# Kernel tuning notes

Measured on AMD Instinct MI355X. Metric: run time of the kernel, lower is better.

## Reference

```python
import jax, jax.numpy as jnp
import numpy as np

EMBED_DIM = 1024
SEQ_LEN = 4096
NUM_HEADS = 16
HEAD_DIM = EMBED_DIM // NUM_HEADS
FREQ_BINS = SEQ_LEN // 2 + 1  # 2049
LN_EPS = 1e-5


def setup_inputs() -> dict:
    key = jax.random.key(0)
    ks = jax.random.split(key, 12)
    B = 4
    x = jax.random.normal(ks[0], (B, SEQ_LEN, EMBED_DIM), dtype=jnp.float32)
    # LayerNorm affine params
    ln_w = jnp.ones((EMBED_DIM,), dtype=jnp.float32)
    ln_b = jnp.zeros((EMBED_DIM,), dtype=jnp.float32)
    # spectral base filter / bias: (H, freq_bins, 1)
    base_filter = jax.random.normal(ks[1], (NUM_HEADS, FREQ_BINS, 1), dtype=jnp.float32)
    base_bias = jax.random.normal(ks[2], (NUM_HEADS, FREQ_BINS, 1), dtype=jnp.float32) - 0.1
    # adaptive MLP (depth=2, width=embed_dim): D -> D -> D -> H*freq*2, relu hidden
    out_size = NUM_HEADS * FREQ_BINS * 2
    s0 = 1.0 / np.sqrt(EMBED_DIM)
    w0 = jax.random.uniform(ks[3], (EMBED_DIM, EMBED_DIM), jnp.float32, -s0, s0)
    b0 = jax.random.uniform(ks[4], (EMBED_DIM,), jnp.float32, -s0, s0)
    w1 = jax.random.uniform(ks[5], (EMBED_DIM, EMBED_DIM), jnp.float32, -s0, s0)
    b1 = jax.random.uniform(ks[6], (EMBED_DIM,), jnp.float32, -s0, s0)
    w2 = jax.random.uniform(ks[7], (EMBED_DIM, out_size), jnp.float32, -s0, s0)
    b2 = jax.random.uniform(ks[8], (out_size,), jnp.float32, -s0, s0)
    return {"x": x, "ln_w": ln_w, "ln_b": ln_b,
            "base_filter": base_filter, "base_bias": base_bias,
            "w0": w0, "b0": b0, "w1": w1, "b1": b1, "w2": w2, "b2": b2}


def _complex_activation(z):
    mag = jnp.abs(z)
    scale = jax.nn.gelu(mag) / (mag + 1e-6)
    return z * scale


def reference(x, ln_w, ln_b, base_filter, base_bias, w0, b0, w1, b1, w2, b2):
    B, N, D = x.shape  # N == SEQ_LEN, D == EMBED_DIM
    # pre-norm LayerNorm over last dim
    mu = x.mean(axis=-1, keepdims=True)
    var = x.var(axis=-1, keepdims=True)
    x_norm = (x - mu) / jnp.sqrt(var + LN_EPS) * ln_w + ln_b
    # split heads: (B, H, N, head_dim)
    x_heads = x_norm.reshape(B, N, NUM_HEADS, HEAD_DIM).transpose(0, 2, 1, 3)
    F_fft = jnp.fft.rfft(x_heads, axis=2)  # (B, H, freq, head_dim), complex
    # adaptive params from mean-pooled context
    context = x_norm.mean(axis=1)  # (B, D)
    h = jax.nn.relu(context @ w0 + b0)
    h = jax.nn.relu(h @ w1 + b1)
    adapt = h @ w2 + b2  # (B, H*freq*2)
    adapt = adapt.reshape(B, NUM_HEADS, FREQ_BINS, 2)
    adaptive_scale = adapt[..., 0:1]
    adaptive_bias = adapt[..., 1:2]
    effective_filter = base_filter * (1.0 + adaptive_scale)  # (B, H, freq, 1)
    effective_bias = base_bias + adaptive_bias
    F_mod = F_fft * effective_filter + effective_bias
    F_nl = _complex_activation(F_mod)
    x_filt = jnp.fft.irfft(F_nl, n=SEQ_LEN, axis=2)  # (B, H, N, head_dim)
    x_filt = x_filt.transpose(0, 2, 1, 3).reshape(B, SEQ_LEN, EMBED_DIM)
    return x_filt  # dropout is identity (inference / rate 0)
```

## Files before the change

kernel.cpp:

```cpp
#include <hip/hip_runtime.h>
#include <hip/hip_fp16.h>
#include <math.h>

#define B_ 4
#define N_ 4096
#define D_ 1024
#define H_ 16
#define HD_ 64
#define FB_ 2049

typedef unsigned short ushort_t;
typedef unsigned int uint_t;

__device__ __forceinline__ float2 cmul(float2 a, float2 b) {
    return make_float2(a.x*b.x - a.y*b.y, a.x*b.y + a.y*b.x);
}
__device__ __forceinline__ float2 cadd(float2 a, float2 b){return make_float2(a.x+b.x,a.y+b.y);}
__device__ __forceinline__ float2 csub(float2 a, float2 b){return make_float2(a.x-b.x,a.y-b.y);}
__device__ __forceinline__ float2 cconj(float2 a){return make_float2(a.x,-a.y);}
__device__ __forceinline__ float2 addi(float2 a, float2 b){return make_float2(a.x-b.y, a.y+b.x);}
__device__ __forceinline__ float2 subi(float2 a, float2 b){return make_float2(a.x+b.y, a.y-b.x);}

__device__ __forceinline__ float gelu_t(float m) {
    float u = 0.7978845608028654f * (m + 0.044715f * m * m * m);
    float e = __expf(-2.0f * u);
    float th = (1.0f - e) / (1.0f + e);
    return 0.5f * m * (1.0f + th);
}
__device__ __forceinline__ float2 cact(float2 z) {
    float m = sqrtf(z.x*z.x + z.y*z.y);
    float s = gelu_t(m) / (m + 1e-6f);
    return make_float2(z.x*s, z.y*s);
}

__device__ __forceinline__ ushort_t f2h(float f) {
    __half h = __float2half_rn(f);
    return *reinterpret_cast<ushort_t*>(&h);
}
__device__ __forceinline__ float h2f(ushort_t u) {
    __half h = *reinterpret_cast<__half*>(&u);
    return __half2float(h);
}
__device__ __forceinline__ uint_t pk2(float a, float b) {
    return (uint_t)f2h(a) | ((uint_t)f2h(b) << 16);
}
__device__ __forceinline__ float lo_f(uint_t u){ return h2f((ushort_t)(u & 0xffffu)); }
__device__ __forceinline__ float hi_f(uint_t u){ return h2f((ushort_t)(u >> 16)); }

#define IX(e) ((e) + ((e) >> 4))

__device__ __forceinline__ int rev12(int p) {
    return ((p & 7) << 9) | (((p >> 3) & 7) << 6) | (((p >> 6) & 7) << 3) | ((p >> 9) & 7);
}

__global__ __launch_bounds__(256) void k_normT(const float* __restrict__ x,
                                               const float* __restrict__ lnw,
                                               const float* __restrict__ lnb,
                                               ushort_t* __restrict__ xt,
                                               float* __restrict__ cpart) {
    __shared__ ushort_t lds16[32 * 1032];
    uint_t* lds32 = (uint_t*)lds16;
    int blk = blockIdx.x;
    int b = blk >> 7, chunk = blk & 127;
    int n0 = chunk << 5;
    int lane = threadIdx.x & 63, w = threadIdx.x >> 6;
    const float4* lw4 = (const float4*)lnw;
    const float4* lb4 = (const float4*)lnb;
    float4 W0 = lw4[lane], W1 = lw4[lane+64], W2 = lw4[lane+128], W3 = lw4[lane+192];
    float4 G0 = lb4[lane], G1 = lb4[lane+64], G2 = lb4[lane+128], G3 = lb4[lane+192];

    for (int j = 0; j < 8; j++) {
        int r = (w << 3) + j;
        const float4* xr = (const float4*)(x + ((size_t)b * N_ + n0 + r) * D_);
        float4 v0 = xr[lane], v1 = xr[lane+64], v2 = xr[lane+128], v3 = xr[lane+192];
        float s = v0.x+v0.y+v0.z+v0.w + v1.x+v1.y+v1.z+v1.w
                + v2.x+v2.y+v2.z+v2.w + v3.x+v3.y+v3.z+v3.w;
        float q = v0.x*v0.x+v0.y*v0.y+v0.z*v0.z+v0.w*v0.w
                + v1.x*v1.x+v1.y*v1.y+v1.z*v1.z+v1.w*v1.w
                + v2.x*v2.x+v2.y*v2.y+v2.z*v2.z+v2.w*v2.w
                + v3.x*v3.x+v3.y*v3.y+v3.z*v3.z+v3.w*v3.w;
        for (int o = 1; o < 64; o <<= 1) { s += __shfl_xor(s, o); q += __shfl_xor(q, o); }
        float mu = s * (1.0f / D_);
        float rstd = rsqrtf(q * (1.0f / D_) - mu * mu + 1e-5f);
        int base = r * 516 + 2 * lane;
        lds32[base]       = pk2((v0.x-mu)*rstd*W0.x+G0.x, (v0.y-mu)*rstd*W0.y+G0.y);
        lds32[base + 1]   = pk2((v0.z-mu)*rstd*W0.z+G0.z, (v0.w-mu)*rstd*W0.w+G0.w);
        lds32[base + 128] = pk2((v1.x-mu)*rstd*W1.x+G1.x, (v1.y-mu)*rstd*W1.y+G1.y);
        lds32[base + 129] = pk2((v1.z-mu)*rstd*W1.z+G1.z, (v1.w-mu)*rstd*W1.w+G1.w);
        lds32[base + 256] = pk2((v2.x-mu)*rstd*W2.x+G2.x, (v2.y-mu)*rstd*W2.y+G2.y);
        lds32[base + 257] = pk2((v2.z-mu)*rstd*W2.z+G2.z, (v2.w-mu)*rstd*W2.w+G2.w);
        lds32[base + 384] = pk2((v3.x-mu)*rstd*W3.x+G3.x, (v3.y-mu)*rstd*W3.y+G3.y);
        lds32[base + 385] = pk2((v3.z-mu)*rstd*W3.z+G3.z, (v3.w-mu)*rstd*W3.w+G3.w);
    }
    __syncthreads();
    for (int half = 0; half < 2; half++) {
        int dp = threadIdx.x + (half << 8);
        float cs_e = 0.f, cs_o = 0.f;
        uint_t ce[16], co[16];
        #pragma unroll
        for (int i = 0; i < 16; i++) {
            uint_t w0 = lds32[(2*i) * 516 + dp];
            uint_t w1 = lds32[(2*i+1) * 516 + dp];
            ce[i] = (w0 & 0xffffu) | (w1 << 16);
            co[i] = (w0 >> 16) | (w1 & 0xffff0000u);
            cs_e += lo_f(w0) + lo_f(w1);
            cs_o += hi_f(w0) + hi_f(w1);
        }
        int de = dp * 2;
        uint4* dste = (uint4*)(xt + ((size_t)(b * 1024 + de)) * 4096 + n0);
        dste[0] = make_uint4(ce[0], ce[1], ce[2], ce[3]);
        dste[1] = make_uint4(ce[4], ce[5], ce[6], ce[7]);
        dste[2] = make_uint4(ce[8], ce[9], ce[10], ce[11]);
        dste[3] = make_uint4(ce[12], ce[13], ce[14], ce[15]);
        uint4* dsto = (uint4*)(xt + ((size_t)(b * 1024 + de + 1)) * 4096 + n0);
        dsto[0] = make_uint4(co[0], co[1], co[2], co[3]);
        dsto[1] = make_uint4(co[4], co[5], co[6], co[7]);
        dsto[2] = make_uint4(co[8], co[9], co[10], co[11]);
        dsto[3] = make_uint4(co[12], co[13], co[14], co[15]);
        ((float2*)(cpart + ((size_t)(b * 128 + chunk)) * D_))[dp] = make_float2(cs_e, cs_o);
    }
}

__global__ __launch_bounds__(256) void k_ctx(const float* __restrict__ cpart,
                                             float* __restrict__ ctx) {
    int id = blockIdx.x * 256 + threadIdx.x;
    int b = id >> 10, d = id & 1023;
    float s = 0.f;
    const float* p = cpart + (size_t)b * 128 * D_ + d;
    #pragma unroll 8
    for (int g = 0; g < 128; g++) s += p[g * D_];
    ctx[id] = s * (1.0f / N_);
}

__global__ __launch_bounds__(256) void k_mlp_part(const float* __restrict__ in,
                                                  const float* __restrict__ w,
                                                  float* __restrict__ part) {
    __shared__ float li[4 * 64];
    int ks = blockIdx.y;
    if (threadIdx.x < 256) {
        int i = threadIdx.x;
        int b = i >> 6, kk = i & 63;
        li[i] = in[b * 1024 + ks * 64 + kk];
    }
    __syncthreads();
    int col = blockIdx.x * 64 + (threadIdx.x & 63);
    int b = threadIdx.x >> 6;
    const float* wp = w + (size_t)(ks * 64) * 1024 + col;
    const float* ip = li + b * 64;
    float a0 = 0.f, a1 = 0.f, a2 = 0.f, a3 = 0.f;
    #pragma unroll
    for (int k = 0; k < 64; k += 4) {
        a0 = fmaf(ip[k],     wp[(size_t)k * 1024],        a0);
        a1 = fmaf(ip[k + 1], wp[(size_t)(k + 1) * 1024],  a1);
        a2 = fmaf(ip[k + 2], wp[(size_t)(k + 2) * 1024],  a2);
        a3 = fmaf(ip[k + 3], wp[(size_t)(k + 3) * 1024],  a3);
    }
    part[((size_t)ks * 4 + b) * 1024 + col] = (a0 + a1) + (a2 + a3);
}

__global__ __launch_bounds__(256) void k_mlp_part2(const float* __restrict__ part,
                                                   const float* __restrict__ bias,
                                                   const float* __restrict__ w,
                                                   float* __restrict__ part2) {
    __shared__ float li[4 * 64];
    int ks = blockIdx.y;
    if (threadIdx.x < 256) {
        int i = threadIdx.x;
        int b = i >> 6, kk = ks * 64 + (i & 63);
        float v = bias[kk];
        #pragma unroll
        for (int s = 0; s < 16; s++) v += part[((size_t)s * 4 + b) * 1024 + kk];
        li[i] = fmaxf(v, 0.f);
    }
    __syncthreads();
    int col = blockIdx.x * 64 + (threadIdx.x & 63);
    int b = threadIdx.x >> 6;
    const float* wp = w + (size_t)(ks * 64) * 1024 + col;
    const float* ip = li + b * 64;
    float a0 = 0.f, a1 = 0.f, a2 = 0.f, a3 = 0.f;
    #pragma unroll
    for (int k = 0; k < 64; k += 4) {
        a0 = fmaf(ip[k],     wp[(size_t)k * 1024],        a0);
        a1 = fmaf(ip[k + 1], wp[(size_t)(k + 1) * 1024],  a1);
        a2 = fmaf(ip[k + 2], wp[(size_t)(k + 2) * 1024],  a2);
        a3 = fmaf(ip[k + 3], wp[(size_t)(k + 3) * 1024],  a3);
    }
    part2[((size_t)ks * 4 + b) * 1024 + col] = (a0 + a1) + (a2 + a3);
}

__global__ __launch_bounds__(256) void k_adapt_part(const float* __restrict__ part2,
                                                    const float* __restrict__ b1,
                                                    const float* __restrict__ w2,
                                                    float* __restrict__ part3) {
    __shared__ float lh[4 * 128];
    int ks = blockIdx.y;
    for (int i = threadIdx.x; i < 512; i += 256) {
        int b = i >> 7, kk = (i & 127) + ks * 128;
        float v = b1[kk];
        #pragma unroll
        for (int s = 0; s < 16; s++) v += part2[((size_t)s * 4 + b) * 1024 + kk];
        lh[i] = fmaxf(v, 0.f);
    }
    __syncthreads();
    int j4 = blockIdx.x * 1024 + threadIdx.x * 4;
    if (j4 < 65568) {
        float a0x=0,a0y=0,a0z=0,a0w=0, a1x=0,a1y=0,a1z=0,a1w=0;
        float a2x=0,a2y=0,a2z=0,a2w=0, a3x=0,a3y=0,a3z=0,a3w=0;
        const float* wp = w2 + (size_t)(ks * 128) * 65568 + j4;
        #pragma unroll 4
        for (int k = 0; k < 128; k++) {
            float4 wv = *(const float4*)(wp + (size_t)k * 65568);
            float h0 = lh[k], h1 = lh[128 + k], h2 = lh[256 + k], h3 = lh[384 + k];
            a0x = fmaf(h0, wv.x, a0x); a0y = fmaf(h0, wv.y, a0y);
            a0z = fmaf(h0, wv.z, a0z); a0w = fmaf(h0, wv.w, a0w);
            a1x = fmaf(h1, wv.x, a1x); a1y = fmaf(h1, wv.y, a1y);
            a1z = fmaf(h1, wv.z, a1z); a1w = fmaf(h1, wv.w, a1w);
            a2x = fmaf(h2, wv.x, a2x); a2y = fmaf(h2, wv.y, a2y);
            a2z = fmaf(h2, wv.z, a2z); a2w = fmaf(h2, wv.w, a2w);
            a3x = fmaf(h3, wv.x, a3x); a3y = fmaf(h3, wv.y, a3y);
            a3z = fmaf(h3, wv.z, a3z); a3w = fmaf(h3, wv.w, a3w);
        }
        float* p3 = part3 + (size_t)ks * 4 * 65568 + j4;
        *(float4*)(p3)              = make_float4(a0x, a0y, a0z, a0w);
        *(float4*)(p3 + 65568)      = make_float4(a1x, a1y, a1z, a1w);
        *(float4*)(p3 + 2 * 65568)  = make_float4(a2x, a2y, a2z, a2w);
        *(float4*)(p3 + 3 * 65568)  = make_float4(a3x, a3y, a3z, a3w);
    }
}

__global__ __launch_bounds__(256) void k_eff(const float* __restrict__ part3,
                                             const float* __restrict__ b2,
                                             const float* __restrict__ bfilt,
                                             const float* __restrict__ bbias,
                                             float2* __restrict__ eff) {
    int p = blockIdx.x * 256 + threadIdx.x;
    if (p >= 32784) return;
    int h = p / 2049, f = p % 2049;
    float bf = bfilt[p], bb = bbias[p];
    float sc0 = b2[2 * p], bi0 = b2[2 * p + 1];
    #pragma unroll
    for (int b = 0; b < 4; b++) {
        float sc = sc0, bi = bi0;
        #pragma unroll
        for (int s = 0; s < 8; s++) {
            const float* q = part3 + ((size_t)s * 4 + b) * 65568 + 2 * p;
            sc += q[0]; bi += q[1];
        }
        eff[((size_t)b * H_ + h) * FB_ + f] = make_float2(bf * (1.0f + sc), bb + bi);
    }
}

template<int M, int SH, bool TW>
__device__ __forceinline__ void dif_stage(float2* buf, const float2* tw, int t) {
    const float s2 = 0.70710678118654752f;
    int j = t & (M - 1);
    int base = 8 * t - 7 * j;
    float2 u0 = buf[IX(base)];
    float2 u1 = buf[IX(base + M)];
    float2 u2 = buf[IX(base + 2*M)];
    float2 u3 = buf[IX(base + 3*M)];
    float2 u4 = buf[IX(base + 4*M)];
    float2 u5 = buf[IX(base + 5*M)];
    float2 u6 = buf[IX(base + 6*M)];
    float2 u7 = buf[IX(base + 7*M)];
    float2 a0 = cadd(u0,u4), a1 = csub(u0,u4), a2 = cadd(u2,u6), a3 = csub(u2,u6);
    float2 E0 = cadd(a0,a2), E1 = subi(a1,a3), E2 = csub(a0,a2), E3 = addi(a1,a3);
    float2 c0 = cadd(u1,u5), c1 = csub(u1,u5), c2 = cadd(u3,u7), c3 = csub(u3,u7);
    float2 O0 = cadd(c0,c2), O1 = subi(c1,c3), O2 = csub(c0,c2), O3 = addi(c1,c3);
    float2 R1 = make_float2(s2*(O1.x + O1.y), s2*(O1.y - O1.x));
    float2 R2 = make_float2(O2.y, -O2.x);
    float2 R3 = make_float2(s2*(O3.y - O3.x), -s2*(O3.x + O3.y));
    float2 X0 = cadd(E0,O0), X4 = csub(E0,O0);
    float2 X1 = cadd(E1,R1), X5 = csub(E1,R1);
    float2 X2 = cadd(E2,R2), X6 = csub(E2,R2);
    float2 X3 = cadd(E3,R3), X7 = csub(E3,R3);
    buf[IX(base)] = X0;
    if (TW) {
        float2 w1 = tw[IX(j << SH)];
        float2 w = w1;
        buf[IX(base + M)]   = cmul(w, X1); w = cmul(w, w1);
        buf[IX(base + 2*M)] = cmul(w, X2); w = cmul(w, w1);
        buf[IX(base + 3*M)] = cmul(w, X3); w = cmul(w, w1);
        buf[IX(base + 4*M)] = cmul(w, X4); w = cmul(w, w1);
        buf[IX(base + 5*M)] = cmul(w, X5); w = cmul(w, w1);
        buf[IX(base + 6*M)] = cmul(w, X6); w = cmul(w, w1);
        buf[IX(base + 7*M)] = cmul(w, X7);
    } else {
        buf[IX(base + M)]   = X1;
        buf[IX(base + 2*M)] = X2;
        buf[IX(base + 3*M)] = X3;
        buf[IX(base + 4*M)] = X4;
        buf[IX(base + 5*M)] = X5;
        buf[IX(base + 6*M)] = X6;
        buf[IX(base + 7*M)] = X7;
    }
}

template<int M, int SH, bool TW>
__device__ __forceinline__ void dit_stage(float2* buf, const float2* tw, int t) {
    const float s2 = 0.70710678118654752f;
    int j = t & (M - 1);
    int base = 8 * t - 7 * j;
    float2 u0 = buf[IX(base)];
    float2 u1, u2, u3, u4, u5, u6, u7;
    if (TW) {
        float2 w1 = cconj(tw[IX(j << SH)]);
        float2 w = w1;
        u1 = cmul(w, buf[IX(base + M)]);   w = cmul(w, w1);
        u2 = cmul(w, buf[IX(base + 2*M)]); w = cmul(w, w1);
        u3 = cmul(w, buf[IX(base + 3*M)]); w = cmul(w, w1);
        u4 = cmul(w, buf[IX(base + 4*M)]); w = cmul(w, w1);
        u5 = cmul(w, buf[IX(base + 5*M)]); w = cmul(w, w1);
        u6 = cmul(w, buf[IX(base + 6*M)]); w = cmul(w, w1);
        u7 = cmul(w, buf[IX(base + 7*M)]);
    } else {
        u1 = buf[IX(base + M)];
        u2 = buf[IX(base + 2*M)];
        u3 = buf[IX(base + 3*M)];
        u4 = buf[IX(base + 4*M)];
        u5 = buf[IX(base + 5*M)];
        u6 = buf[IX(base + 6*M)];
        u7 = buf[IX(base + 7*M)];
    }
    float2 a0 = cadd(u0,u4), a1 = csub(u0,u4), a2 = cadd(u2,u6), a3 = csub(u2,u6);
    float2 E0 = cadd(a0,a2), E1 = addi(a1,a3), E2 = csub(a0,a2), E3 = subi(a1,a3);
    float2 c0 = cadd(u1,u5), c1 = csub(u1,u5), c2 = cadd(u3,u7), c3 = csub(u3,u7);
    float2 O0 = cadd(c0,c2), O1 = addi(c1,c3), O2 = csub(c0,c2), O3 = subi(c1,c3);
    float2 R1 = make_float2(s2*(O1.x - O1.y),  s2*(O1.x + O1.y));
    float2 R2 = make_float2(-O2.y, O2.x);
    float2 R3 = make_float2(-s2*(O3.x + O3.y), s2*(O3.x - O3.y));
    buf[IX(base)]       = cadd(E0,O0);
    buf[IX(base + 4*M)] = csub(E0,O0);
    buf[IX(base + M)]   = cadd(E1,R1);
    buf[IX(base + 5*M)] = csub(E1,R1);
    buf[IX(base + 2*M)] = cadd(E2,R2);
    buf[IX(base + 6*M)] = csub(E2,R2);
    buf[IX(base + 3*M)] = cadd(E3,R3);
    buf[IX(base + 7*M)] = csub(E3,R3);
}

__global__ __launch_bounds__(512, 6) void k_fftmod(ushort_t* __restrict__ xt,
                                                   const float2* __restrict__ eff) {
    __shared__ float2 buf[4352];
    __shared__ float2 tw[544];
    int t = threadIdx.x;
    int sig0 = blockIdx.x * 2;
    int b = sig0 >> 10;
    int h = (sig0 & 1023) >> 6;
    const float2* ef = eff + ((size_t)b * H_ + h) * FB_;
    ushort_t* xs = xt + (size_t)sig0 * 4096;

    {
        float sv, cv;
        __sincosf(-(float)M_PI * (float)t * (1.0f / 2048.0f), &sv, &cv);
        tw[IX(t)] = make_float2(cv, sv);
    }
    {
        const uint4* pa = (const uint4*)xs;
        const uint4* pb = pa + 512;
        uint4 ua = pa[t], ub = pb[t];
        int n = t << 3;
        buf[IX(n+0)] = make_float2(lo_f(ua.x), lo_f(ub.x));
        buf[IX(n+1)] = make_float2(hi_f(ua.x), hi_f(ub.x));
        buf[IX(n+2)] = make_float2(lo_f(ua.y), lo_f(ub.y));
        buf[IX(n+3)] = make_float2(hi_f(ua.y), hi_f(ub.y));
        buf[IX(n+4)] = make_float2(lo_f(ua.z), lo_f(ub.z));
        buf[IX(n+5)] = make_float2(hi_f(ua.z), hi_f(ub.z));
        buf[IX(n+6)] = make_float2(lo_f(ua.w), lo_f(ub.w));
        buf[IX(n+7)] = make_float2(hi_f(ua.w), hi_f(ub.w));
    }
    __syncthreads();

    dif_stage<512, 0, true >(buf, tw, t); __syncthreads();
    dif_stage<64,  3, true >(buf, tw, t); __syncthreads();
    dif_stage<8,   6, true >(buf, tw, t); __syncthreads();
    dif_stage<1,   0, false>(buf, tw, t); __syncthreads();

    if (t == 0) {
        float2 Z = buf[IX(0)];
        float2 e0 = ef[0];
        float Av = Z.x * e0.x + e0.y;
        float Bv = Z.y * e0.x + e0.y;
        float ma = fabsf(Av); Av *= gelu_t(ma) / (ma + 1e-6f);
        float mb = fabsf(Bv); Bv *= gelu_t(mb) / (mb + 1e-6f);
        buf[IX(0)] = make_float2(Av, Bv);
    }
    #pragma unroll
    for (int ii = 0; ii < 4; ii++) {
        int k = 1 + t + (ii << 9);
        if (k == 2048) {
            float2 Z = buf[IX(4)];
            float2 eN = ef[2048];
            float Av = Z.x * eN.x + eN.y;
            float Bv = Z.y * eN.x + eN.y;
            float ma = fabsf(Av); Av *= gelu_t(ma) / (ma + 1e-6f);
            float mb = fabsf(Bv); Bv *= gelu_t(mb) / (mb + 1e-6f);
            buf[IX(4)] = make_float2(Av, Bv);
        } else {
            int pk = rev12(k);
            int pq = rev12(4096 - k);
            float2 Zk = buf[IX(pk)], Zq = buf[IX(pq)];
            float2 A  = make_float2(0.5f*(Zk.x + Zq.x), 0.5f*(Zk.y - Zq.y));
            float2 Bc = make_float2(0.5f*(Zk.y + Zq.y), 0.5f*(Zq.x - Zk.x));
            float2 e = ef[k];
            float2 Ap = make_float2(A.x * e.x + e.y,  A.y * e.x);
            float2 Bp = make_float2(Bc.x * e.x + e.y, Bc.y * e.x);
            Ap = cact(Ap); Bp = cact(Bp);
            buf[IX(pk)] = make_float2(Ap.x - Bp.y, Ap.y + Bp.x);
            buf[IX(pq)] = make_float2(Ap.x + Bp.y, Bp.x - Ap.y);
        }
    }
    __syncthreads();

    dit_stage<1,   0, false>(buf, tw, t); __syncthreads();
    dit_stage<8,   6, true >(buf, tw, t); __syncthreads();
    dit_stage<64,  3, true >(buf, tw, t); __syncthreads();
    dit_stage<512, 0, true >(buf, tw, t); __syncthreads();

    {
        const float sc = 1.0f / 4096.0f;
        int n = t << 3;
        float2 z0 = buf[IX(n+0)], z1 = buf[IX(n+1)], z2 = buf[IX(n+2)], z3 = buf[IX(n+3)];
        float2 z4 = buf[IX(n+4)], z5 = buf[IX(n+5)], z6 = buf[IX(n+6)], z7 = buf[IX(n+7)];
        uint4 oa, ob;
        oa.x = pk2(z0.x*sc, z1.x*sc); oa.y = pk2(z2.x*sc, z3.x*sc);
        oa.z = pk2(z4.x*sc, z5.x*sc); oa.w = pk2(z6.x*sc, z7.x*sc);
        ob.x = pk2(z0.y*sc, z1.y*sc); ob.y = pk2(z2.y*sc, z3.y*sc);
        ob.z = pk2(z4.y*sc, z5.y*sc); ob.w = pk2(z6.y*sc, z7.y*sc);
        ((uint4*)xs)[t] = oa;
        ((uint4*)xs)[t + 512] = ob;
    }
}

__global__ __launch_bounds__(256) void k_transout(const ushort_t* __restrict__ xt,
                                                  float* __restrict__ out) {
    __shared__ float tile[64 * 65];
    int bid = blockIdx.x;
    int b = bid >> 10;
    int rem = bid & 1023;
    int nt = rem >> 4;
    int dt = rem & 15;
    int n0 = nt << 6;
    int tx = threadIdx.x & 63, ty = threadIdx.x >> 6;
    const ushort_t* xtb = xt + ((size_t)((b * H_ + dt) * HD_)) * (size_t)N_ + n0;
    for (int r = 0; r < 16; r++) {
        int dloc = ty + 4 * r;
        tile[dloc * 65 + tx] = h2f(xtb[(size_t)dloc * N_ + tx]);
    }
    __syncthreads();
    float* ob = out + ((size_t)b * N_ + n0) * D_ + dt * HD_;
    for (int r = 0; r < 16; r++) {
        int nn = ty + 4 * r;
        ob[(size_t)nn * D_ + tx] = tile[tx * 65 + nn];
    }
}

extern "C" void kernel_launch(void* const* d_in, const int* in_sizes, int n_in,
                              void* d_out, int out_size, void* d_ws, size_t ws_size,
                              hipStream_t stream) {
    const float* x     = (const float*)d_in[0];
    const float* lnw   = (const float*)d_in[1];
    const float* lnb   = (const float*)d_in[2];
    const float* bfilt = (const float*)d_in[3];
    const float* bbias = (const float*)d_in[4];
    const float* w0    = (const float*)d_in[5];
    const float* b0    = (const float*)d_in[6];
    const float* w1    = (const float*)d_in[7];
    const float* b1    = (const float*)d_in[8];
    const float* w2    = (const float*)d_in[9];
    const float* b2    = (const float*)d_in[10];

    float* ws = (float*)d_ws;
    ushort_t* xt   = (ushort_t*)ws;
    float*  cpart  = ws + 8388608;
    float*  ctx    = ws + 8912896;
    float*  pA     = ws + 8916992;
    float*  pB     = ws + 8982528;
    float*  p3     = ws + 9048064;
    float2* eff    = (float2*)(ws + 11146240);
    float*  out    = (float*)d_out;

    k_normT     <<<512,  256, 0, stream>>>(x, lnw, lnb, xt, cpart);
    k_ctx       <<<16,   256, 0, stream>>>(cpart, ctx);
    k_mlp_part  <<<dim3(16, 16), 256, 0, stream>>>(ctx, w0, pA);
    k_mlp_part2 <<<dim3(16, 16), 256, 0, stream>>>(pA, b0, w1, pB);
    k_adapt_part<<<dim3(65, 8), 256, 0, stream>>>(pB, b1, w2, p3);
    k_eff       <<<129,  256, 0, stream>>>(p3, b2, bfilt, bbias, eff);
    k_fftmod    <<<2048, 512, 0, stream>>>(xt, eff);
    k_transout  <<<4096, 256, 0, stream>>>(xt, out);
}
```

Measured before the change: 183.1 us.

## Switch 4096-point FFT from radix-8 to radix-16 stages with 256 threads

Replaces the four radix-8 forward and inverse FFT stages with three radix-16 stages, cutting one LDS round-trip and one barrier per direction. Blocks shrink from 512 to 256 threads, and each thread now handles 16 elements, loads and stores two uint4 per plane, and computes two twiddle-table entries. The digit-reversal mapping changes to base 16 to match. The cost is higher register pressure per thread and possibly lower occupancy, with launch bounds now set to (256,4).

Result: no change. 183.5 us (+0.2%).

```diff
diff --git a/kernel.cpp b/kernel.cpp
--- a/kernel.cpp
+++ b/kernel.cpp
@@ -49,8 +49,8 @@
 
 #define IX(e) ((e) + ((e) >> 4))
 
-__device__ __forceinline__ int rev12(int p) {
-    return ((p & 7) << 9) | (((p >> 3) & 7) << 6) | (((p >> 6) & 7) << 3) | ((p >> 9) & 7);
+__device__ __forceinline__ int rev16(int p) {
+    return ((p & 15) << 8) | (p & 240) | ((p >> 8) & 15);
 }
 
 __global__ __launch_bounds__(256) void k_normT(const float* __restrict__ x,
@@ -250,96 +250,124 @@
     }
 }
 
-template<int M, int SH, bool TW>
-__device__ __forceinline__ void dif_stage(float2* buf, const float2* tw, int t) {
+template<int M, int SC, bool TW>
+__device__ __forceinline__ void dif16(float2* buf, const float2* tw, int t) {
+    const float c1 = 0.92387953251128675f, s1 = 0.38268343236508977f;
     const float s2 = 0.70710678118654752f;
     int j = t & (M - 1);
-    int base = 8 * t - 7 * j;
-    float2 u0 = buf[IX(base)];
-    float2 u1 = buf[IX(base + M)];
-    float2 u2 = buf[IX(base + 2*M)];
-    float2 u3 = buf[IX(base + 3*M)];
-    float2 u4 = buf[IX(base + 4*M)];
-    float2 u5 = buf[IX(base + 5*M)];
-    float2 u6 = buf[IX(base + 6*M)];
-    float2 u7 = buf[IX(base + 7*M)];
-    float2 a0 = cadd(u0,u4), a1 = csub(u0,u4), a2 = cadd(u2,u6), a3 = csub(u2,u6);
-    float2 E0 = cadd(a0,a2), E1 = subi(a1,a3), E2 = csub(a0,a2), E3 = addi(a1,a3);
-    float2 c0 = cadd(u1,u5), c1 = csub(u1,u5), c2 = cadd(u3,u7), c3 = csub(u3,u7);
-    float2 O0 = cadd(c0,c2), O1 = subi(c1,c3), O2 = csub(c0,c2), O3 = addi(c1,c3);
-    float2 R1 = make_float2(s2*(O1.x + O1.y), s2*(O1.y - O1.x));
-    float2 R2 = make_float2(O2.y, -O2.x);
-    float2 R3 = make_float2(s2*(O3.y - O3.x), -s2*(O3.x + O3.y));
-    float2 X0 = cadd(E0,O0), X4 = csub(E0,O0);
-    float2 X1 = cadd(E1,R1), X5 = csub(E1,R1);
-    float2 X2 = cadd(E2,R2), X6 = csub(E2,R2);
-    float2 X3 = cadd(E3,R3), X7 = csub(E3,R3);
-    buf[IX(base)] = X0;
+    int base = 16 * t - 15 * j;
+    float2 u[16];
+    #pragma unroll
+    for (int k = 0; k < 16; k++) u[k] = buf[IX(base + k * M)];
+    float2 A[4][4];
+    #pragma unroll
+    for (int b = 0; b < 4; b++) {
+        float2 t0 = cadd(u[b], u[b+8]),  t1 = csub(u[b], u[b+8]);
+        float2 t2 = cadd(u[b+4], u[b+12]), t3 = csub(u[b+4], u[b+12]);
+        A[b][0] = cadd(t0, t2);
+        A[b][1] = subi(t1, t3);
+        A[b][2] = csub(t0, t2);
+        A[b][3] = addi(t1, t3);
+    }
+    const float2 W1 = make_float2(c1, -s1), W2c = make_float2(s2, -s2), W3 = make_float2(s1, -c1);
+    const float2 W4 = make_float2(0.f, -1.f), W6 = make_float2(-s2, -s2), W9 = make_float2(-c1, s1);
+    A[1][1] = cmul(A[1][1], W1);  A[1][2] = cmul(A[1][2], W2c); A[1][3] = cmul(A[1][3], W3);
+    A[2][1] = cmul(A[2][1], W2c); A[2][2] = cmul(A[2][2], W4);  A[2][3] = cmul(A[2][3], W6);
+    A[3][1] = cmul(A[3][1], W3);  A[3][2] = cmul(A[3][2], W6);  A[3][3] = cmul(A[3][3], W9);
+    float2 X[16];
+    #pragma unroll
+    for (int c = 0; c < 4; c++) {
+        float2 t0 = cadd(A[0][c], A[2][c]), t1 = csub(A[0][c], A[2][c]);
+        float2 t2 = cadd(A[1][c], A[3][c]), t3 = csub(A[1][c], A[3][c]);
+        X[c]      = cadd(t0, t2);
+        X[c + 4]  = subi(t1, t3);
+        X[c + 8]  = csub(t0, t2);
+        X[c + 12] = addi(t1, t3);
+    }
+    buf[IX(base)] = X[0];
     if (TW) {
-        float2 w1 = tw[IX(j << SH)];
-        float2 w = w1;
-        buf[IX(base + M)]   = cmul(w, X1); w = cmul(w, w1);
-        buf[IX(base + 2*M)] = cmul(w, X2); w = cmul(w, w1);
-        buf[IX(base + 3*M)] = cmul(w, X3); w = cmul(w, w1);
-        buf[IX(base + 4*M)] = cmul(w, X4); w = cmul(w, w1);
-        buf[IX(base + 5*M)] = cmul(w, X5); w = cmul(w, w1);
-        buf[IX(base + 6*M)] = cmul(w, X6); w = cmul(w, w1);
-        buf[IX(base + 7*M)] = cmul(w, X7);
+        float2 w2 = tw[IX(2 * SC * j)];
+        float2 wa = tw[IX(SC * j)];
+        float2 wb = w2;
+        buf[IX(base + M)]      = cmul(wa, X[1]);
+        buf[IX(base + 2 * M)]  = cmul(wb, X[2]);
+        wa = cmul(wa, w2); buf[IX(base + 3 * M)]  = cmul(wa, X[3]);
+        wb = cmul(wb, w2); buf[IX(base + 4 * M)]  = cmul(wb, X[4]);
+        wa = cmul(wa, w2); buf[IX(base + 5 * M)]  = cmul(wa, X[5]);
+        wb = cmul(wb, w2); buf[IX(base + 6 * M)]  = cmul(wb, X[6]);
+        wa = cmul(wa, w2); buf[IX(base + 7 * M)]  = cmul(wa, X[7]);
+        wb = cmul(wb, w2); buf[IX(base + 8 * M)]  = cmul(wb, X[8]);
+        wa = cmul(wa, w2); buf[IX(base + 9 * M)]  = cmul(wa, X[9]);
+        wb = cmul(wb, w2); buf[IX(base + 10 * M)] = cmul(wb, X[10]);
+        wa = cmul(wa, w2); buf[IX(base + 11 * M)] = cmul(wa, X[11]);
+        wb = cmul(wb, w2); buf[IX(base + 12 * M)] = cmul(wb, X[12]);
+        wa = cmul(wa, w2); buf[IX(base + 13 * M)] = cmul(wa, X[13]);
+        wb = cmul(wb, w2); buf[IX(base + 14 * M)] = cmul(wb, X[14]);
+        wa = cmul(wa, w2); buf[IX(base + 15 * M)] = cmul(wa, X[15]);
     } else {
-        buf[IX(base + M)]   = X1;
-        buf[IX(base + 2*M)] = X2;
-        buf[IX(base + 3*M)] = X3;
-        buf[IX(base + 4*M)] = X4;
-        buf[IX(base + 5*M)] = X5;
-        buf[IX(base + 6*M)] = X6;
-        buf[IX(base + 7*M)] = X7;
-    }
-}
-
-template<int M, int SH, bool TW>
-__device__ __forceinline__ void dit_stage(float2* buf, const float2* tw, int t) {
+        #pragma unroll
+        for (int k = 1; k < 16; k++) buf[IX(base + k * M)] = X[k];
+    }
+}
+
+template<int M, int SC, bool TW>
+__device__ __forceinline__ void dit16(float2* buf, const float2* tw, int t) {
+    const float c1 = 0.92387953251128675f, s1 = 0.38268343236508977f;
     const float s2 = 0.70710678118654752f;
     int j = t & (M - 1);
-    int base = 8 * t - 7 * j;
-    float2 u0 = buf[IX(base)];
-    float2 u1, u2, u3, u4, u5, u6, u7;
+    int base = 16 * t - 15 * j;
+    float2 u[16];
+    u[0] = buf[IX(base)];
     if (TW) {
-        float2 w1 = cconj(tw[IX(j << SH)]);
-        float2 w = w1;
-        u1 = cmul(w, buf[IX(base + M)]);   w = cmul(w, w1);
-        u2 = cmul(w, buf[IX(base + 2*M)]); w = cmul(w, w1);
-        u3 = cmul(w, buf[IX(base + 3*M)]); w = cmul(w, w1);
-        u4 = cmul(w, buf[IX(base + 4*M)]); w = cmul(w, w1);
-        u5 = cmul(w, buf[IX(base + 5*M)]); w = cmul(w, w1);
-        u6 = cmul(w, buf[IX(base + 6*M)]); w = cmul(w, w1);
-        u7 = cmul(w, buf[IX(base + 7*M)]);
+        float2 w2 = cconj(tw[IX(2 * SC * j)]);
+        float2 wa = cconj(tw[IX(SC * j)]);
+        float2 wb = w2;
+        u[1]  = cmul(wa, buf[IX(base + M)]);
+        u[2]  = cmul(wb, buf[IX(base + 2 * M)]);
+        wa = cmul(wa, w2); u[3]  = cmul(wa, buf[IX(base + 3 * M)]);
+        wb = cmul(wb, w2); u[4]  = cmul(wb, buf[IX(base + 4 * M)]);
+        wa = cmul(wa, w2); u[5]  = cmul(wa, buf[IX(base + 5 * M)]);
+        wb = cmul(wb, w2); u[6]  = cmul(wb, buf[IX(base + 6 * M)]);
+        wa = cmul(wa, w2); u[7]  = cmul(wa, buf[IX(base + 7 * M)]);
+        wb = cmul(wb, w2); u[8]  = cmul(wb, buf[IX(base + 8 * M)]);
+        wa = cmul(wa, w2); u[9]  = cmul(wa, buf[IX(base + 9 * M)]);
+        wb = cmul(wb, w2); u[10] = cmul(wb, buf[IX(base + 10 * M)]);
+        wa = cmul(wa, w2); u[11] = cmul(wa, buf[IX(base + 11 * M)]);
+        wb = cmul(wb, w2); u[12] = cmul(wb, buf[IX(base + 12 * M)]);
+        wa = cmul(wa, w2); u[13] = cmul(wa, buf[IX(base + 13 * M)]);
+        wb = cmul(wb, w2); u[14] = cmul(wb, buf[IX(base + 14 * M)]);
+        wa = cmul(wa, w2); u[15] = cmul(wa, buf[IX(base + 15 * M)]);
     } else {
-        u1 = buf[IX(base + M)];
-        u2 = buf[IX(base + 2*M)];
-        u3 = buf[IX(base + 3*M)];
-        u4 = buf[IX(base + 4*M)];
-        u5 = buf[IX(base + 5*M)];
-        u6 = buf[IX(base + 6*M)];
-        u7 = buf[IX(base + 7*M)];
-    }
-    float2 a0 = cadd(u0,u4), a1 = csub(u0,u4), a2 = cadd(u2,u6), a3 = csub(u2,u6);
-    float2 E0 = cadd(a0,a2), E1 = addi(a1,a3), E2 = csub(a0,a2), E3 = subi(a1,a3);
-    float2 c0 = cadd(u1,u5), c1 = csub(u1,u5), c2 = cadd(u3,u7), c3 = csub(u3,u7);
-    float2 O0 = cadd(c0,c2), O1 = addi(c1,c3), O2 = csub(c0,c2), O3 = subi(c1,c3);
-    float2 R1 = make_float2(s2*(O1.x - O1.y),  s2*(O1.x + O1.y));
-    float2 R2 = make_float2(-O2.y, O2.x);
-    float2 R3 = make_float2(-s2*(O3.x + O3.y), s2*(O3.x - O3.y));
-    buf[IX(base)]       = cadd(E0,O0);
-    buf[IX(base + 4*M)] = csub(E0,O0);
-    buf[IX(base + M)]   = cadd(E1,R1);
-    buf[IX(base + 5*M)] = csub(E1,R1);
-    buf[IX(base + 2*M)] = cadd(E2,R2);
-    buf[IX(base + 6*M)] = csub(E2,R2);
-    buf[IX(base + 3*M)] = cadd(E3,R3);
-    buf[IX(base + 7*M)] = csub(E3,R3);
-}
-
-__global__ __launch_bounds__(512, 6) void k_fftmod(ushort_t* __restrict__ xt,
+        #pragma unroll
+        for (int k = 1; k < 16; k++) u[k] = buf[IX(base + k * M)];
+    }
+    float2 A[4][4];
+    #pragma unroll
+    for (int b = 0; b < 4; b++) {
+        float2 t0 = cadd(u[b], u[b+8]),  t1 = csub(u[b], u[b+8]);
+        float2 t2 = cadd(u[b+4], u[b+12]), t3 = csub(u[b+4], u[b+12]);
+        A[b][0] = cadd(t0, t2);
+        A[b][1] = addi(t1, t3);
+        A[b][2] = csub(t0, t2);
+        A[b][3] = subi(t1, t3);
+    }
+    const float2 W1 = make_float2(c1, s1), W2c = make_float2(s2, s2), W3 = make_float2(s1, c1);
+    const float2 W4 = make_float2(0.f, 1.f), W6 = make_float2(-s2, s2), W9 = make_float2(-c1, -s1);
+    A[1][1] = cmul(A[1][1], W1);  A[1][2] = cmul(A[1][2], W2c); A[1][3] = cmul(A[1][3], W3);
+    A[2][1] = cmul(A[2][1], W2c); A[2][2] = cmul(A[2][2], W4);  A[2][3] = cmul(A[2][3], W6);
+    A[3][1] = cmul(A[3][1], W3);  A[3][2] = cmul(A[3][2], W6);  A[3][3] = cmul(A[3][3], W9);
+    #pragma unroll
+    for (int c = 0; c < 4; c++) {
+        float2 t0 = cadd(A[0][c], A[2][c]), t1 = csub(A[0][c], A[2][c]);
+        float2 t2 = cadd(A[1][c], A[3][c]), t3 = csub(A[1][c], A[3][c]);
+        buf[IX(base + c * M)]        = cadd(t0, t2);
+        buf[IX(base + (c + 4) * M)]  = addi(t1, t3);
+        buf[IX(base + (c + 8) * M)]  = csub(t0, t2);
+        buf[IX(base + (c + 12) * M)] = subi(t1, t3);
+    }
+}
+
+__global__ __launch_bounds__(256, 4) void k_fftmod(ushort_t* __restrict__ xt,
                                                    const float2* __restrict__ eff) {
     __shared__ float2 buf[4352];
     __shared__ float2 tw[544];
@@ -350,31 +378,41 @@
     const float2* ef = eff + ((size_t)b * H_ + h) * FB_;
     ushort_t* xs = xt + (size_t)sig0 * 4096;
 
-    {
+    #pragma unroll
+    for (int ii = 0; ii < 2; ii++) {
+        int e = t + (ii << 8);
         float sv, cv;
-        __sincosf(-(float)M_PI * (float)t * (1.0f / 2048.0f), &sv, &cv);
-        tw[IX(t)] = make_float2(cv, sv);
+        __sincosf(-(float)M_PI * (float)e * (1.0f / 2048.0f), &sv, &cv);
+        tw[IX(e)] = make_float2(cv, sv);
     }
     {
         const uint4* pa = (const uint4*)xs;
         const uint4* pb = pa + 512;
-        uint4 ua = pa[t], ub = pb[t];
-        int n = t << 3;
-        buf[IX(n+0)] = make_float2(lo_f(ua.x), lo_f(ub.x));
-        buf[IX(n+1)] = make_float2(hi_f(ua.x), hi_f(ub.x));
-        buf[IX(n+2)] = make_float2(lo_f(ua.y), lo_f(ub.y));
-        buf[IX(n+3)] = make_float2(hi_f(ua.y), hi_f(ub.y));
-        buf[IX(n+4)] = make_float2(lo_f(ua.z), lo_f(ub.z));
-        buf[IX(n+5)] = make_float2(hi_f(ua.z), hi_f(ub.z));
-        buf[IX(n+6)] = make_float2(lo_f(ua.w), lo_f(ub.w));
-        buf[IX(n+7)] = make_float2(hi_f(ua.w), hi_f(ub.w));
-    }
-    __syncthreads();
-
-    dif_stage<512, 0, true >(buf, tw, t); __syncthreads();
-    dif_stage<64,  3, true >(buf, tw, t); __syncthreads();
-    dif_stage<8,   6, true >(buf, tw, t); __syncthreads();
-    dif_stage<1,   0, false>(buf, tw, t); __syncthreads();
+        uint4 a0 = pa[2*t], a1 = pa[2*t+1];
+        uint4 b0 = pb[2*t], b1 = pb[2*t+1];
+        int n = t << 4;
+        buf[IX(n+0)]  = make_float2(lo_f(a0.x), lo_f(b0.x));
+        buf[IX(n+1)]  = make_float2(hi_f(a0.x), hi_f(b0.x));
+        buf[IX(n+2)]  = make_float2(lo_f(a0.y), lo_f(b0.y));
+        buf[IX(n+3)]  = make_float2(hi_f(a0.y), hi_f(b0.y));
+        buf[IX(n+4)]  = make_float2(lo_f(a0.z), lo_f(b0.z));
+        buf[IX(n+5)]  = make_float2(hi_f(a0.z), hi_f(b0.z));
+        buf[IX(n+6)]  = make_float2(lo_f(a0.w), lo_f(b0.w));
+        buf[IX(n+7)]  = make_float2(hi_f(a0.w), hi_f(b0.w));
+        buf[IX(n+8)]  = make_float2(lo_f(a1.x), lo_f(b1.x));
+        buf[IX(n+9)]  = make_float2(hi_f(a1.x), hi_f(b1.x));
+        buf[IX(n+10)] = make_float2(lo_f(a1.y), lo_f(b1.y));
+        buf[IX(n+11)] = make_float2(hi_f(a1.y), hi_f(b1.y));
+        buf[IX(n+12)] = make_float2(lo_f(a1.z), lo_f(b1.z));
+        buf[IX(n+13)] = make_float2(hi_f(a1.z), hi_f(b1.z));
+        buf[IX(n+14)] = make_float2(lo_f(a1.w), lo_f(b1.w));
+        buf[IX(n+15)] = make_float2(hi_f(a1.w), hi_f(b1.w));
+    }
+    __syncthreads();
+
+    dif16<256, 1,  true >(buf, tw, t); __syncthreads();
+    dif16<16,  16, true >(buf, tw, t); __syncthreads();
+    dif16<1,   1,  false>(buf, tw, t); __syncthreads();
 
     if (t == 0) {
         float2 Z = buf[IX(0)];
@@ -386,19 +424,19 @@
         buf[IX(0)] = make_float2(Av, Bv);
     }
     #pragma unroll
-    for (int ii = 0; ii < 4; ii++) {
-        int k = 1 + t + (ii << 9);
+    for (int ii = 0; ii < 8; ii++) {
+        int k = 1 + t + (ii << 8);
         if (k == 2048) {
-            float2 Z = buf[IX(4)];
+            float2 Z = buf[IX(8)];
             float2 eN = ef[2048];
             float Av = Z.x * eN.x + eN.y;
             float Bv = Z.y * eN.x + eN.y;
             float ma = fabsf(Av); Av *= gelu_t(ma) / (ma + 1e-6f);
             float mb = fabsf(Bv); Bv *= gelu_t(mb) / (mb + 1e-6f);
-            buf[IX(4)] = make_float2(Av, Bv);
+            buf[IX(8)] = make_float2(Av, Bv);
         } else {
-            int pk = rev12(k);
-            int pq = rev12(4096 - k);
+            int pk = rev16(k);
+            int pq = rev16(4096 - k);
             float2 Zk = buf[IX(pk)], Zq = buf[IX(pq)];
             float2 A  = make_float2(0.5f*(Zk.x + Zq.x), 0.5f*(Zk.y - Zq.y));
             float2 Bc = make_float2(0.5f*(Zk.y + Zq.y), 0.5f*(Zq.x - Zk.x));
@@ -412,23 +450,30 @@
     }
     __syncthreads();
 
-    dit_stage<1,   0, false>(buf, tw, t); __syncthreads();
-    dit_stage<8,   6, true >(buf, tw, t); __syncthreads();
-    dit_stage<64,  3, true >(buf, tw, t); __syncthreads();
-    dit_stage<512, 0, true >(buf, tw, t); __syncthreads();
+    dit16<1,   1,  false>(buf, tw, t); __syncthreads();
+    dit16<16,  16, true >(buf, tw, t); __syncthreads();
+    dit16<256, 1,  true >(buf, tw, t); __syncthreads();
 
     {
         const float sc = 1.0f / 4096.0f;
-        int n = t << 3;
-        float2 z0 = buf[IX(n+0)], z1 = buf[IX(n+1)], z2 = buf[IX(n+2)], z3 = buf[IX(n+3)];
-        float2 z4 = buf[IX(n+4)], z5 = buf[IX(n+5)], z6 = buf[IX(n+6)], z7 = buf[IX(n+7)];
-        uint4 oa, ob;
-        oa.x = pk2(z0.x*sc, z1.x*sc); oa.y = pk2(z2.x*sc, z3.x*sc);
-        oa.z = pk2(z4.x*sc, z5.x*sc); oa.w = pk2(z6.x*sc, z7.x*sc);
-        ob.x = pk2(z0.y*sc, z1.y*sc); ob.y = pk2(z2.y*sc, z3.y*sc);
-        ob.z = pk2(z4.y*sc, z5.y*sc); ob.w = pk2(z6.y*sc, z7.y*sc);
-        ((uint4*)xs)[t] = oa;
-        ((uint4*)xs)[t + 512] = ob;
+        int n = t << 4;
+        uint4 oa0, oa1, ob0, ob1;
+        float2 z0 = buf[IX(n+0)],  z1 = buf[IX(n+1)],  z2 = buf[IX(n+2)],  z3 = buf[IX(n+3)];
+        float2 z4 = buf[IX(n+4)],  z5 = buf[IX(n+5)],  z6 = buf[IX(n+6)],  z7 = buf[IX(n+7)];
+        oa0.x = pk2(z0.x*sc, z1.x*sc); oa0.y = pk2(z2.x*sc, z3.x*sc);
+        oa0.z = pk2(z4.x*sc, z5.x*sc); oa0.w = pk2(z6.x*sc, z7.x*sc);
+        ob0.x = pk2(z0.y*sc, z1.y*sc); ob0.y = pk2(z2.y*sc, z3.y*sc);
+        ob0.z = pk2(z4.y*sc, z5.y*sc); ob0.w = pk2(z6.y*sc, z7.y*sc);
+        float2 y0 = buf[IX(n+8)],  y1 = buf[IX(n+9)],  y2 = buf[IX(n+10)], y3 = buf[IX(n+11)];
+        float2 y4 = buf[IX(n+12)], y5 = buf[IX(n+13)], y6 = buf[IX(n+14)], y7 = buf[IX(n+15)];
+        oa1.x = pk2(y0.x*sc, y1.x*sc); oa1.y = pk2(y2.x*sc, y3.x*sc);
+        oa1.z = pk2(y4.x*sc, y5.x*sc); oa1.w = pk2(y6.x*sc, y7.x*sc);
+        ob1.x = pk2(y0.y*sc, y1.y*sc); ob1.y = pk2(y2.y*sc, y3.y*sc);
+        ob1.z = pk2(y4.y*sc, y5.y*sc); ob1.w = pk2(y6.y*sc, y7.y*sc);
+        uint4* pa = (uint4*)xs;
+        uint4* pb = pa + 512;
+        pa[2*t] = oa0; pa[2*t+1] = oa1;
+        pb[2*t] = ob0; pb[2*t+1] = ob1;
     }
 }
 
@@ -486,6 +531,6 @@
     k_mlp_part2 <<<dim3(16, 16), 256, 0, stream>>>(pA, b0, w1, pB);
     k_adapt_part<<<dim3(65, 8), 256, 0, stream>>>(pB, b1, w2, p3);
     k_eff       <<<129,  256, 0, stream>>>(p3, b2, bfilt, bbias, eff);
-    k_fftmod    <<<2048, 512, 0, stream>>>(xt, eff);
+    k_fftmod    <<<2048, 256, 0, stream>>>(xt, eff);
     k_transout  <<<4096, 256, 0, stream>>>(xt, out);
 }
```
